# Kernel tuning notes

Hardware: AMD Instinct MI355X
Metric: run time of the kernel (lower is better)

Reference implementation:

```python
import jax, jax.numpy as jnp
import numpy as np

# dims
N = 200000   # n_nodes
D = 256      # node_dim
S = 8        # n_substructures
M = 100000   # gathered atom indices per substructure (flattened detections)
H = 64       # dim_per_substructure
B = 4096     # batch_size (max(batch_idx)+1)


def setup_inputs() -> dict:
    key = jax.random.key(0)
    ks = jax.random.split(key, 8)
    node_features = jax.random.normal(ks[0], (N, D), dtype=jnp.float32)
    sub_indices = jax.random.randint(ks[1], (S, M), 0, N, dtype=jnp.int32)
    batch_idx = jax.random.randint(ks[2], (N,), 0, B, dtype=jnp.int32)
    # per-substructure MLP params: Linear(D,H) -> ReLU -> Linear(H,H)
    s1 = 1.0 / np.sqrt(D)
    s2 = 1.0 / np.sqrt(H)
    W1 = jax.random.uniform(ks[3], (S, D, H), minval=-s1, maxval=s1, dtype=jnp.float32)
    b1 = jax.random.uniform(ks[4], (S, H), minval=-s1, maxval=s1, dtype=jnp.float32)
    W2 = jax.random.uniform(ks[5], (S, H, H), minval=-s2, maxval=s2, dtype=jnp.float32)
    b2 = jax.random.uniform(ks[6], (S, H), minval=-s2, maxval=s2, dtype=jnp.float32)
    return {"node_features": node_features, "W1": W1, "b1": b1, "W2": W2,
            "b2": b2, "sub_indices": sub_indices, "batch_idx": batch_idx}


def reference(node_features, W1, b1, W2, b2, sub_indices, batch_idx):
    # gather node feats per substructure: [S, M, D]
    gathered = node_features[sub_indices]
    # 2-layer MLP per substructure (sum aggregation path of the module)
    h = jax.nn.relu(jnp.einsum('smd,sdh->smh', gathered, W1) + b1[:, None, :])
    enc = jnp.einsum('smh,shk->smk', h, W2) + b2[:, None, :]   # [S, M, H]
    # scatter-add into per-graph slots (index_add_ over batch idx of gathered atoms)
    seg = batch_idx[sub_indices]                               # [S, M]
    agg = jax.vmap(lambda e, s: jax.ops.segment_sum(e, s, num_segments=B))(enc, seg)  # [S, B, H]
    # concatenate per-substructure blocks -> [B, S*H]
    return jnp.transpose(agg, (1, 0, 2)).reshape(B, S * H)
```

## Files before the change

### kernel.cpp

```cpp
#include <hip/hip_runtime.h>

#define Nn 200000
#define Dn 256
#define Hn 64
#define Sn 8
#define Mn 100000
#define Bn 4096

#define RPB 256
#define KC 32
#define NT 256
#define XS 40
#define WS 40

typedef __attribute__((ext_vector_type(8))) short bf16x8;
typedef __attribute__((ext_vector_type(4))) float f32x4;

static __device__ __forceinline__ void split2(float a, float b,
                                              unsigned& h, unsigned& l) {
    unsigned ua = __float_as_uint(a), ub = __float_as_uint(b);
    unsigned ha = ua & 0xFFFF0000u, hb = ub & 0xFFFF0000u;
    float la = a - __uint_as_float(ha);
    float lb = b - __uint_as_float(hb);
    h = (ua >> 16) | hb;
    l = (__float_as_uint(la) >> 16) | (__float_as_uint(lb) & 0xFFFF0000u);
}

__global__ __launch_bounds__(NT, 3)
void l1_kernel(const float* __restrict__ nf, const float* __restrict__ W1,
               const float* __restrict__ b1, const int* __restrict__ sub_idx,
               const int* __restrict__ bidx, float* __restrict__ hsum,
               float* __restrict__ cnt)
{
    __shared__ __align__(16) unsigned short Xhi[RPB * XS];
    __shared__ __align__(16) unsigned short Xlo[RPB * XS];
    __shared__ __align__(16) unsigned short Whi[Hn * WS];
    __shared__ __align__(16) unsigned short Wlo[Hn * WS];
    __shared__ unsigned short sseg[RPB];

    const int s    = blockIdx.y;
    const int m0   = blockIdx.x * RPB;
    const int tid  = threadIdx.x;
    const int lane = tid & 63;
    const int w    = tid >> 6;
    const int qq   = lane >> 4;
    const int r16  = lane & 15;

    const int  m    = m0 + tid;
    const bool val  = (m < Mn);
    const int  node = val ? sub_idx[(size_t)s * Mn + m] : 0;
    sseg[tid] = (unsigned short)(val ? bidx[node] : 0);

    const float* xrow = nf + (size_t)node * Dn;

    const int wc = tid & 63;
    const int wq = tid >> 6;

    f32x4 acc[4][4];
#pragma unroll
    for (int mi = 0; mi < 4; ++mi)
#pragma unroll
        for (int ni = 0; ni < 4; ++ni) acc[mi][ni] = (f32x4){0.f, 0.f, 0.f, 0.f};

    float fx[8 * 4];
    float fw[8];

    {
        const float4* xp = (const float4*)xrow;
#pragma unroll
        for (int v = 0; v < 8; ++v) *(float4*)&fx[4 * v] = xp[v];
        const float* wp = W1 + ((size_t)(s * Dn + 8 * wq)) * Hn + wc;
#pragma unroll
        for (int i = 0; i < 8; ++i) fw[i] = wp[(size_t)i * Hn];
    }

    for (int c = 0; c < Dn / KC; ++c) {
        __syncthreads();

#pragma unroll
        for (int v = 0; v < 4; ++v) {
            unsigned h[4], l[4];
#pragma unroll
            for (int j = 0; j < 4; ++j)
                split2(fx[8 * v + 2 * j], fx[8 * v + 2 * j + 1], h[j], l[j]);
            *(uint4*)&Xhi[tid * XS + 8 * v] = make_uint4(h[0], h[1], h[2], h[3]);
            *(uint4*)&Xlo[tid * XS + 8 * v] = make_uint4(l[0], l[1], l[2], l[3]);
        }
        {
            unsigned h[4], l[4];
#pragma unroll
            for (int j = 0; j < 4; ++j) split2(fw[2 * j], fw[2 * j + 1], h[j], l[j]);
            *(uint4*)&Whi[wc * WS + 8 * wq] = make_uint4(h[0], h[1], h[2], h[3]);
            *(uint4*)&Wlo[wc * WS + 8 * wq] = make_uint4(l[0], l[1], l[2], l[3]);
        }
        __syncthreads();

        if (c + 1 < Dn / KC) {
            const int kk = (c + 1) * KC;
            const float4* xp = (const float4*)(xrow + kk);
#pragma unroll
            for (int v = 0; v < 8; ++v) *(float4*)&fx[4 * v] = xp[v];
            const float* wp = W1 + ((size_t)(s * Dn + kk + 8 * wq)) * Hn + wc;
#pragma unroll
            for (int i = 0; i < 8; ++i) fw[i] = wp[(size_t)i * Hn];
        }

        bf16x8 ah[4], al[4];
#pragma unroll
        for (int mi = 0; mi < 4; ++mi) {
            const int rb = (64 * w + 16 * mi + r16) * XS + 8 * qq;
            ah[mi] = *(const bf16x8*)&Xhi[rb];
            al[mi] = *(const bf16x8*)&Xlo[rb];
        }
#pragma unroll
        for (int ni = 0; ni < 4; ++ni) {
            const int cb = (16 * ni + r16) * WS + 8 * qq;
            bf16x8 bh = *(const bf16x8*)&Whi[cb];
            bf16x8 bl = *(const bf16x8*)&Wlo[cb];
#pragma unroll
            for (int mi = 0; mi < 4; ++mi)
                acc[mi][ni] = __builtin_amdgcn_mfma_f32_16x16x32_bf16(ah[mi], bh, acc[mi][ni], 0, 0, 0);
#pragma unroll
            for (int mi = 0; mi < 4; ++mi)
                acc[mi][ni] = __builtin_amdgcn_mfma_f32_16x16x32_bf16(ah[mi], bl, acc[mi][ni], 0, 0, 0);
#pragma unroll
            for (int mi = 0; mi < 4; ++mi)
                acc[mi][ni] = __builtin_amdgcn_mfma_f32_16x16x32_bf16(al[mi], bh, acc[mi][ni], 0, 0, 0);
        }
    }

    float bcol[4];
#pragma unroll
    for (int ni = 0; ni < 4; ++ni) bcol[ni] = b1[s * Hn + 16 * ni + r16];

#pragma unroll
    for (int mi = 0; mi < 4; ++mi) {
#pragma unroll
        for (int r = 0; r < 4; ++r) {
            const int row = 64 * w + 16 * mi + 4 * qq + r;
            const int mg  = m0 + row;
            if (mg >= Mn) continue;
            const int sg = sseg[row];
            float* dst = hsum + ((size_t)(s * Bn + sg)) * Hn;
#pragma unroll
            for (int ni = 0; ni < 4; ++ni) {
                float v = fmaxf(acc[mi][ni][r] + bcol[ni], 0.f);
                atomicAdd(dst + 16 * ni + r16, v);
            }
        }
    }
    if (val) atomicAdd(cnt + s * Bn + sseg[tid], 1.0f);
}

__global__ __launch_bounds__(256)
void l2_kernel(const float* __restrict__ hsum, const float* __restrict__ cnt,
               const float* __restrict__ W2, const float* __restrict__ b2,
               float* __restrict__ out)
{
    __shared__ float W2s[Hn * Hn];
    const int s    = blockIdx.y;
    const int b0   = blockIdx.x * 64;
    const int tid  = threadIdx.x;
    const int lane = tid & 63;
    const int w    = tid >> 6;

    const float* w2g = W2 + (size_t)s * Hn * Hn;
#pragma unroll
    for (int i = 0; i < 4; ++i)
        ((float4*)W2s)[tid + 256 * i] = ((const float4*)w2g)[tid + 256 * i];
    __syncthreads();

    const float b2v = b2[s * Hn + lane];

#pragma unroll
    for (int g = 0; g < 4; ++g) {
        const int rb = b0 + w * 16 + g * 4;
        float hv[4], ct[4], acc[4];
#pragma unroll
        for (int i = 0; i < 4; ++i) {
            const size_t rr = (size_t)s * Bn + rb + i;
            hv[i]  = hsum[rr * Hn + lane];
            ct[i]  = cnt[rr];
            acc[i] = 0.f;
        }
#pragma unroll 8
        for (int j = 0; j < Hn; ++j) {
            float wv = W2s[j * Hn + lane];
#pragma unroll
            for (int i = 0; i < 4; ++i)
                acc[i] = fmaf(__shfl(hv[i], j), wv, acc[i]);
        }
#pragma unroll
        for (int i = 0; i < 4; ++i)
            out[(size_t)(rb + i) * (Sn * Hn) + s * Hn + lane] = acc[i] + ct[i] * b2v;
    }
}

extern "C" void kernel_launch(void* const* d_in, const int* in_sizes, int n_in,
                              void* d_out, int out_size, void* d_ws, size_t ws_size,
                              hipStream_t stream)
{
    const float* nf   = (const float*)d_in[0];
    const float* W1   = (const float*)d_in[1];
    const float* b1   = (const float*)d_in[2];
    const float* W2   = (const float*)d_in[3];
    const float* b2   = (const float*)d_in[4];
    const int*   sidx = (const int*)d_in[5];
    const int*   bidx = (const int*)d_in[6];
    float* out = (float*)d_out;

    float* hsum = (float*)d_ws;
    float* cnt  = hsum + (size_t)Sn * Bn * Hn;

    hipMemsetAsync(d_ws, 0, ((size_t)Sn * Bn * Hn + (size_t)Sn * Bn) * sizeof(float),
                   stream);

    dim3 g1((Mn + RPB - 1) / RPB, Sn);
    l1_kernel<<<g1, NT, 0, stream>>>(nf, W1, b1, sidx, bidx, hsum, cnt);

    dim3 g2(Bn / 64, Sn);
    l2_kernel<<<g2, 256, 0, stream>>>(hsum, cnt, W2, b2, out);
}
```

Baseline: 536.2 us.

## Sort gathered rows by segment and reduce in shared memory instead of global atomics

Adds histogram, scan and scatter kernels that bucket the gathered atoms by (substructure, graph) segment. Each L1 block then handles 8 consecutive segments, accumulates its ReLU outputs with shared-memory atomics and writes hsum once, with no global float atomics. Counts now come from the bucket offsets, so the count atomics and most of the memset go away. The cost is three extra launches, a single-block scan, and chunks that are partly empty when a group of segments does not fill 256 rows, which wastes MFMA work.

```diff
diff --git a/kernel.cpp b/kernel.cpp
--- a/kernel.cpp
+++ b/kernel.cpp
@@ -10,8 +10,11 @@
 #define RPB 256
 #define KC 32
 #define NT 256
+#define VB 8
 #define XS 40
 #define WS 40
+
+#define NBIN (Sn * Bn)
 
 typedef __attribute__((ext_vector_type(8))) short bf16x8;
 typedef __attribute__((ext_vector_type(4))) float f32x4;
@@ -26,134 +29,206 @@
     l = (__float_as_uint(la) >> 16) | (__float_as_uint(lb) & 0xFFFF0000u);
 }
 
+__global__ __launch_bounds__(256)
+void hist_kernel(const int* __restrict__ sidx, const int* __restrict__ bidx,
+                 unsigned* __restrict__ hist)
+{
+    const int s = blockIdx.y;
+    const int m = blockIdx.x * 256 + threadIdx.x;
+    if (m < Mn) {
+        const int node = sidx[(size_t)s * Mn + m];
+        const int sg   = bidx[node];
+        atomicAdd(&hist[s * Bn + sg], 1u);
+    }
+}
+
+__global__ __launch_bounds__(1024)
+void scan_kernel(const unsigned* __restrict__ hist, unsigned* __restrict__ bstart,
+                 unsigned* __restrict__ cursor)
+{
+    __shared__ unsigned part[1024];
+    const int tid  = threadIdx.x;
+    const int base = tid * 32;
+    unsigned vals[32], sum = 0;
+#pragma unroll
+    for (int j = 0; j < 32; ++j) { vals[j] = hist[base + j]; sum += vals[j]; }
+    part[tid] = sum;
+    __syncthreads();
+    for (int d = 1; d < 1024; d <<= 1) {
+        unsigned t = (tid >= d) ? part[tid - d] : 0u;
+        __syncthreads();
+        part[tid] += t;
+        __syncthreads();
+    }
+    unsigned off = part[tid] - sum;
+#pragma unroll
+    for (int j = 0; j < 32; ++j) {
+        bstart[base + j] = off;
+        cursor[base + j] = off;
+        off += vals[j];
+    }
+    if (tid == 1023) bstart[NBIN] = off;
+}
+
+__global__ __launch_bounds__(256)
+void scatter_kernel(const int* __restrict__ sidx, const int* __restrict__ bidx,
+                    unsigned* __restrict__ cursor, unsigned* __restrict__ order)
+{
+    const int s = blockIdx.y;
+    const int m = blockIdx.x * 256 + threadIdx.x;
+    if (m < Mn) {
+        const int node = sidx[(size_t)s * Mn + m];
+        const int sg   = bidx[node];
+        const unsigned pos = atomicAdd(&cursor[s * Bn + sg], 1u);
+        order[pos] = ((unsigned)sg << 18) | (unsigned)node;
+    }
+}
+
 __global__ __launch_bounds__(NT, 3)
 void l1_kernel(const float* __restrict__ nf, const float* __restrict__ W1,
-               const float* __restrict__ b1, const int* __restrict__ sub_idx,
-               const int* __restrict__ bidx, float* __restrict__ hsum,
-               float* __restrict__ cnt)
+               const float* __restrict__ b1, const unsigned* __restrict__ order,
+               const unsigned* __restrict__ bstart, float* __restrict__ hsum)
 {
     __shared__ __align__(16) unsigned short Xhi[RPB * XS];
     __shared__ __align__(16) unsigned short Xlo[RPB * XS];
     __shared__ __align__(16) unsigned short Whi[Hn * WS];
     __shared__ __align__(16) unsigned short Wlo[Hn * WS];
-    __shared__ unsigned short sseg[RPB];
+    __shared__ unsigned short rowlb[RPB];
+    __shared__ float hacc[VB * Hn];
 
     const int s    = blockIdx.y;
-    const int m0   = blockIdx.x * RPB;
+    const int b0   = blockIdx.x * VB;
     const int tid  = threadIdx.x;
     const int lane = tid & 63;
     const int w    = tid >> 6;
     const int qq   = lane >> 4;
     const int r16  = lane & 15;
-
-    const int  m    = m0 + tid;
-    const bool val  = (m < Mn);
-    const int  node = val ? sub_idx[(size_t)s * Mn + m] : 0;
-    sseg[tid] = (unsigned short)(val ? bidx[node] : 0);
-
-    const float* xrow = nf + (size_t)node * Dn;
-
-    const int wc = tid & 63;
-    const int wq = tid >> 6;
-
-    f32x4 acc[4][4];
-#pragma unroll
-    for (int mi = 0; mi < 4; ++mi)
-#pragma unroll
-        for (int ni = 0; ni < 4; ++ni) acc[mi][ni] = (f32x4){0.f, 0.f, 0.f, 0.f};
-
-    float fx[8 * 4];
-    float fw[8];
-
-    {
-        const float4* xp = (const float4*)xrow;
-#pragma unroll
-        for (int v = 0; v < 8; ++v) *(float4*)&fx[4 * v] = xp[v];
-        const float* wp = W1 + ((size_t)(s * Dn + 8 * wq)) * Hn + wc;
-#pragma unroll
-        for (int i = 0; i < 8; ++i) fw[i] = wp[(size_t)i * Hn];
-    }
-
-    for (int c = 0; c < Dn / KC; ++c) {
+    const int wc   = tid & 63;
+    const int wq   = tid >> 6;
+
+    const int bin0 = s * Bn + b0;
+    const unsigned r0 = bstart[bin0];
+    const unsigned r1 = bstart[bin0 + VB];
+
+    if (tid < (VB * Hn) / 4)
+        ((float4*)hacc)[tid] = make_float4(0.f, 0.f, 0.f, 0.f);
+
+    float bcol[4];
+#pragma unroll
+    for (int ni = 0; ni < 4; ++ni) bcol[ni] = b1[s * Hn + 16 * ni + r16];
+
+    const int nch = (int)((r1 - r0 + RPB - 1) / RPB);
+    for (int ch = 0; ch < nch; ++ch) {
+        const unsigned i  = r0 + (unsigned)ch * RPB + (unsigned)tid;
+        const bool val    = (i < r1);
+        const unsigned e  = val ? order[i] : 0u;
+        const int node    = (int)(e & 0x3FFFFu);
+        const int lb      = (int)(e >> 18) - b0;
+
         __syncthreads();
-
-#pragma unroll
-        for (int v = 0; v < 4; ++v) {
-            unsigned h[4], l[4];
-#pragma unroll
-            for (int j = 0; j < 4; ++j)
-                split2(fx[8 * v + 2 * j], fx[8 * v + 2 * j + 1], h[j], l[j]);
-            *(uint4*)&Xhi[tid * XS + 8 * v] = make_uint4(h[0], h[1], h[2], h[3]);
-            *(uint4*)&Xlo[tid * XS + 8 * v] = make_uint4(l[0], l[1], l[2], l[3]);
-        }
+        rowlb[tid] = val ? (unsigned short)lb : (unsigned short)0xFFFF;
+
+        const float* xrow = nf + (size_t)node * Dn;
+
+        f32x4 acc[4][4];
+#pragma unroll
+        for (int mi = 0; mi < 4; ++mi)
+#pragma unroll
+            for (int ni = 0; ni < 4; ++ni) acc[mi][ni] = (f32x4){0.f, 0.f, 0.f, 0.f};
+
+        float fx[32];
+        float fw[8];
         {
-            unsigned h[4], l[4];
-#pragma unroll
-            for (int j = 0; j < 4; ++j) split2(fw[2 * j], fw[2 * j + 1], h[j], l[j]);
-            *(uint4*)&Whi[wc * WS + 8 * wq] = make_uint4(h[0], h[1], h[2], h[3]);
-            *(uint4*)&Wlo[wc * WS + 8 * wq] = make_uint4(l[0], l[1], l[2], l[3]);
-        }
-        __syncthreads();
-
-        if (c + 1 < Dn / KC) {
-            const int kk = (c + 1) * KC;
-            const float4* xp = (const float4*)(xrow + kk);
-#pragma unroll
-            for (int v = 0; v < 8; ++v) *(float4*)&fx[4 * v] = xp[v];
-            const float* wp = W1 + ((size_t)(s * Dn + kk + 8 * wq)) * Hn + wc;
-#pragma unroll
-            for (int i = 0; i < 8; ++i) fw[i] = wp[(size_t)i * Hn];
-        }
-
-        bf16x8 ah[4], al[4];
+            const float4* xp = (const float4*)xrow;
+#pragma unroll
+            for (int v = 0; v < 8; ++v)
+                *(float4*)&fx[4 * v] = val ? xp[v] : make_float4(0.f, 0.f, 0.f, 0.f);
+            const float* wp = W1 + ((size_t)(s * Dn + 8 * wq)) * Hn + wc;
+#pragma unroll
+            for (int k = 0; k < 8; ++k) fw[k] = wp[(size_t)k * Hn];
+        }
+
+        for (int c = 0; c < Dn / KC; ++c) {
+            __syncthreads();
+
+#pragma unroll
+            for (int v = 0; v < 4; ++v) {
+                unsigned h[4], l[4];
+#pragma unroll
+                for (int j = 0; j < 4; ++j)
+                    split2(fx[8 * v + 2 * j], fx[8 * v + 2 * j + 1], h[j], l[j]);
+                *(uint4*)&Xhi[tid * XS + 8 * v] = make_uint4(h[0], h[1], h[2], h[3]);
+                *(uint4*)&Xlo[tid * XS + 8 * v] = make_uint4(l[0], l[1], l[2], l[3]);
+            }
+            {
+                unsigned h[4], l[4];
+#pragma unroll
+                for (int j = 0; j < 4; ++j) split2(fw[2 * j], fw[2 * j + 1], h[j], l[j]);
+                *(uint4*)&Whi[wc * WS + 8 * wq] = make_uint4(h[0], h[1], h[2], h[3]);
+                *(uint4*)&Wlo[wc * WS + 8 * wq] = make_uint4(l[0], l[1], l[2], l[3]);
+            }
+            __syncthreads();
+
+            if (c + 1 < Dn / KC) {
+                const int kk = (c + 1) * KC;
+                const float4* xp = (const float4*)(xrow + kk);
+#pragma unroll
+                for (int v = 0; v < 8; ++v)
+                    *(float4*)&fx[4 * v] = val ? xp[v] : make_float4(0.f, 0.f, 0.f, 0.f);
+                const float* wp = W1 + ((size_t)(s * Dn + kk + 8 * wq)) * Hn + wc;
+#pragma unroll
+                for (int k = 0; k < 8; ++k) fw[k] = wp[(size_t)k * Hn];
+            }
+
+            bf16x8 ah[4], al[4];
+#pragma unroll
+            for (int mi = 0; mi < 4; ++mi) {
+                const int rb = (64 * w + 16 * mi + r16) * XS + 8 * qq;
+                ah[mi] = *(const bf16x8*)&Xhi[rb];
+                al[mi] = *(const bf16x8*)&Xlo[rb];
+            }
+#pragma unroll
+            for (int ni = 0; ni < 4; ++ni) {
+                const int cb = (16 * ni + r16) * WS + 8 * qq;
+                bf16x8 bh = *(const bf16x8*)&Whi[cb];
+                bf16x8 bl = *(const bf16x8*)&Wlo[cb];
+#pragma unroll
+                for (int mi = 0; mi < 4; ++mi)
+                    acc[mi][ni] = __builtin_amdgcn_mfma_f32_16x16x32_bf16(ah[mi], bh, acc[mi][ni], 0, 0, 0);
+#pragma unroll
+                for (int mi = 0; mi < 4; ++mi)
+                    acc[mi][ni] = __builtin_amdgcn_mfma_f32_16x16x32_bf16(ah[mi], bl, acc[mi][ni], 0, 0, 0);
+#pragma unroll
+                for (int mi = 0; mi < 4; ++mi)
+                    acc[mi][ni] = __builtin_amdgcn_mfma_f32_16x16x32_bf16(al[mi], bh, acc[mi][ni], 0, 0, 0);
+            }
+        }
+
 #pragma unroll
         for (int mi = 0; mi < 4; ++mi) {
-            const int rb = (64 * w + 16 * mi + r16) * XS + 8 * qq;
-            ah[mi] = *(const bf16x8*)&Xhi[rb];
-            al[mi] = *(const bf16x8*)&Xlo[rb];
-        }
-#pragma unroll
-        for (int ni = 0; ni < 4; ++ni) {
-            const int cb = (16 * ni + r16) * WS + 8 * qq;
-            bf16x8 bh = *(const bf16x8*)&Whi[cb];
-            bf16x8 bl = *(const bf16x8*)&Wlo[cb];
-#pragma unroll
-            for (int mi = 0; mi < 4; ++mi)
-                acc[mi][ni] = __builtin_amdgcn_mfma_f32_16x16x32_bf16(ah[mi], bh, acc[mi][ni], 0, 0, 0);
-#pragma unroll
-            for (int mi = 0; mi < 4; ++mi)
-                acc[mi][ni] = __builtin_amdgcn_mfma_f32_16x16x32_bf16(ah[mi], bl, acc[mi][ni], 0, 0, 0);
-#pragma unroll
-            for (int mi = 0; mi < 4; ++mi)
-                acc[mi][ni] = __builtin_amdgcn_mfma_f32_16x16x32_bf16(al[mi], bh, acc[mi][ni], 0, 0, 0);
-        }
-    }
-
-    float bcol[4];
-#pragma unroll
-    for (int ni = 0; ni < 4; ++ni) bcol[ni] = b1[s * Hn + 16 * ni + r16];
-
-#pragma unroll
-    for (int mi = 0; mi < 4; ++mi) {
-#pragma unroll
-        for (int r = 0; r < 4; ++r) {
-            const int row = 64 * w + 16 * mi + 4 * qq + r;
-            const int mg  = m0 + row;
-            if (mg >= Mn) continue;
-            const int sg = sseg[row];
-            float* dst = hsum + ((size_t)(s * Bn + sg)) * Hn;
-#pragma unroll
-            for (int ni = 0; ni < 4; ++ni) {
-                float v = fmaxf(acc[mi][ni][r] + bcol[ni], 0.f);
-                atomicAdd(dst + 16 * ni + r16, v);
-            }
-        }
-    }
-    if (val) atomicAdd(cnt + s * Bn + sseg[tid], 1.0f);
+#pragma unroll
+            for (int r = 0; r < 4; ++r) {
+                const int row = 64 * w + 16 * mi + 4 * qq + r;
+                const int lb2 = rowlb[row];
+                if (lb2 == 0xFFFF) continue;
+#pragma unroll
+                for (int ni = 0; ni < 4; ++ni) {
+                    float v = fmaxf(acc[mi][ni][r] + bcol[ni], 0.f);
+                    atomicAdd(&hacc[lb2 * Hn + 16 * ni + r16], v);
+                }
+            }
+        }
+    }
+
+    __syncthreads();
+    if (tid < (VB * Hn) / 4) {
+        float4 v = ((float4*)hacc)[tid];
+        ((float4*)(hsum + (size_t)bin0 * Hn))[tid] = v;
+    }
 }
 
 __global__ __launch_bounds__(256)
-void l2_kernel(const float* __restrict__ hsum, const float* __restrict__ cnt,
+void l2_kernel(const float* __restrict__ hsum, const unsigned* __restrict__ bstart,
                const float* __restrict__ W2, const float* __restrict__ b2,
                float* __restrict__ out)
 {
@@ -178,9 +253,9 @@
         float hv[4], ct[4], acc[4];
 #pragma unroll
         for (int i = 0; i < 4; ++i) {
-            const size_t rr = (size_t)s * Bn + rb + i;
-            hv[i]  = hsum[rr * Hn + lane];
-            ct[i]  = cnt[rr];
+            const int bin = s * Bn + rb + i;
+            hv[i]  = hsum[(size_t)bin * Hn + lane];
+            ct[i]  = (float)(bstart[bin + 1] - bstart[bin]);
             acc[i] = 0.f;
         }
 #pragma unroll 8
@@ -209,15 +284,22 @@
     const int*   bidx = (const int*)d_in[6];
     float* out = (float*)d_out;
 
-    float* hsum = (float*)d_ws;
-    float* cnt  = hsum + (size_t)Sn * Bn * Hn;
-
-    hipMemsetAsync(d_ws, 0, ((size_t)Sn * Bn * Hn + (size_t)Sn * Bn) * sizeof(float),
-                   stream);
-
-    dim3 g1((Mn + RPB - 1) / RPB, Sn);
-    l1_kernel<<<g1, NT, 0, stream>>>(nf, W1, b1, sidx, bidx, hsum, cnt);
+    float*    hsum   = (float*)d_ws;
+    unsigned* hist   = (unsigned*)(hsum + (size_t)NBIN * Hn);
+    unsigned* bstart = hist + NBIN;
+    unsigned* cursor = bstart + NBIN + 1;
+    unsigned* order  = cursor + NBIN;
+
+    hipMemsetAsync(hist, 0, NBIN * sizeof(unsigned), stream);
+
+    dim3 gm((Mn + 255) / 256, Sn);
+    hist_kernel<<<gm, 256, 0, stream>>>(sidx, bidx, hist);
+    scan_kernel<<<1, 1024, 0, stream>>>(hist, bstart, cursor);
+    scatter_kernel<<<gm, 256, 0, stream>>>(sidx, bidx, cursor, order);
+
+    dim3 g1(Bn / VB, Sn);
+    l1_kernel<<<g1, NT, 0, stream>>>(nf, W1, b1, order, bstart, hsum);
 
     dim3 g2(Bn / 64, Sn);
-    l2_kernel<<<g2, 256, 0, stream>>>(hsum, cnt, W2, b2, out);
-}
+    l2_kernel<<<g2, 256, 0, stream>>>(hsum, bstart, W2, b2, out);
+}
```

After: 791.5 us. 1.48x slower.
